# Kernel optimization log

Measured on AMD Instinct MI355X. Metric: run time of the kernel, lower is better.

## Reference

```python
import jax, jax.numpy as jnp
import numpy as np
import math

DIM = 1024
NUM_HEADS = 16
HEAD_DIM = DIM // NUM_HEADS
B, S = 2, 2048

def setup_inputs() -> dict:
    key = jax.random.key(0)
    ks = jax.random.split(key, 9)
    sc = 0.02
    return {
        "x": jax.random.normal(ks[0], (B, S, DIM), jnp.float32),
        "Wq": jax.random.normal(ks[1], (DIM, DIM), jnp.float32) * sc,
        "bq": jax.random.normal(ks[2], (DIM,), jnp.float32) * sc,
        "Wk": jax.random.normal(ks[3], (DIM, DIM), jnp.float32) * sc,
        "bk": jax.random.normal(ks[4], (DIM,), jnp.float32) * sc,
        "Wv": jax.random.normal(ks[5], (DIM, DIM), jnp.float32) * sc,
        "bv": jax.random.normal(ks[6], (DIM,), jnp.float32) * sc,
        "Wo": jax.random.normal(ks[7], (DIM, DIM), jnp.float32) * sc,
        "bo": jax.random.normal(ks[8], (DIM,), jnp.float32) * sc,
    }

def reference(x, Wq, bq, Wk, bk, Wv, bv, Wo, bo):
    b, s, d = x.shape
    h, hd = NUM_HEADS, HEAD_DIM
    # qkv projections: [B,S,D] -> [B,H,S,hd]
    def split_heads(t):
        return t.reshape(b, s, h, hd).transpose(0, 2, 1, 3)
    q = split_heads(x @ Wq + bq)
    k = split_heads(x @ Wk + bk)
    v = split_heads(x @ Wv + bv)
    # scores [B,H,S,S], scale, causal mask via where(-10000), softmax
    scores = jnp.einsum('bhqd,bhkd->bhqk', q, k) / math.sqrt(hd)
    causal = jnp.tril(jnp.ones((s, s), dtype=bool))  # [S,S]
    scores = jnp.where(causal[None, None], scores, jnp.asarray(-10000.0, scores.dtype))
    probs = jax.nn.softmax(scores, axis=-1)
    ctx = jnp.einsum('bhqk,bhkd->bhqd', probs, v)
    ctx = ctx.transpose(0, 2, 1, 3).reshape(b, s, d)
    return ctx @ Wo + bo
```

## Files before the change

### kernel.cpp

```cpp
#include <hip/hip_runtime.h>
#include <hip/hip_bf16.h>

#define DIM 1024
#define NUM_HEADS 16
#define HEAD_DIM 64
#define BATCH 2
#define SEQ 2048
#define M_ROWS (BATCH * SEQ)

typedef short bh8 __attribute__((ext_vector_type(8)));
typedef float f32x4 __attribute__((ext_vector_type(4)));
typedef float f32x16 __attribute__((ext_vector_type(16)));

#define SCALE_Q 0.18033688011116016f

#define MFMA16(a, b, c) __builtin_amdgcn_mfma_f32_16x16x32_bf16(a, b, c, 0, 0, 0)
#define MFMA32(a, b, c) __builtin_amdgcn_mfma_f32_32x32x16_bf16(a, b, c, 0, 0, 0)

#if __has_builtin(__builtin_amdgcn_exp2f)
#define EXP2F(x) __builtin_amdgcn_exp2f(x)
#else
#define EXP2F(x) exp2f(x)
#endif

__device__ __forceinline__ ushort f2bf(float f) {
    union { float f; unsigned u; } v; v.f = f;
    unsigned u = v.u;
    unsigned r = (u + 0x7FFFu + ((u >> 16) & 1u)) >> 16;
    return (ushort)r;
}

__device__ __forceinline__ unsigned cvt_pk_bf16(float lo, float hi) {
    unsigned r;
    asm("v_cvt_pk_bf16_f32 %0, %1, %2" : "=v"(r) : "v"(lo), "v"(hi));
    return r;
}

__device__ __forceinline__ void plane_swap(unsigned a, unsigned b,
                                           unsigned& o0, unsigned& o1, int h) {
#if __has_builtin(__builtin_amdgcn_permlane32_swap)
    (void)h;
    auto pr = __builtin_amdgcn_permlane32_swap(a, b, false, false);
    unsigned o[2]; __builtin_memcpy(o, &pr, 8);
    o0 = o[0]; o1 = o[1];
#else
    unsigned sa = (unsigned)__shfl_xor((int)a, 32);
    unsigned sb = (unsigned)__shfl_xor((int)b, 32);
    o0 = h ? sb : a;
    o1 = h ? b : sa;
#endif
}

__device__ __forceinline__ void async_cp16(const ushort* g, ushort* l) {
    __builtin_amdgcn_global_load_lds(
        (const __attribute__((address_space(1))) void*)(uintptr_t)g,
        (__attribute__((address_space(3))) void*)(uint32_t)(uintptr_t)l,
        16, 0, 0);
}

__global__ __launch_bounds__(256) void prep_inputs(
    const float* __restrict__ W0, const float* __restrict__ W1,
    const float* __restrict__ W2, const float* __restrict__ W3,
    const float* __restrict__ x,
    ushort* __restrict__ T0, ushort* __restrict__ T1,
    ushort* __restrict__ T2, ushort* __restrict__ T3,
    ushort* __restrict__ xb)
{
    const int z = blockIdx.z;
    const int t = threadIdx.x;
    if (z == 4) {
        int base = (blockIdx.y * 32 + blockIdx.x) * 1024 + t;
        const float4* in4 = (const float4*)x;
        ushort4* out4 = (ushort4*)xb;
        #pragma unroll
        for (int i = 0; i < 4; ++i) {
            float4 v = in4[base + i * 256];
            ushort4 o;
            o.x = f2bf(v.x); o.y = f2bf(v.y); o.z = f2bf(v.z); o.w = f2bf(v.w);
            out4[base + i * 256] = o;
        }
        return;
    }
    __shared__ float tile[32][33];
    const float* W = (z == 0) ? W0 : (z == 1) ? W1 : (z == 2) ? W2 : W3;
    ushort* Wt = (z == 0) ? T0 : (z == 1) ? T1 : (z == 2) ? T2 : T3;
    const int tx = t & 31, ty = t >> 5;
    const int k0 = blockIdx.y * 32, n0 = blockIdx.x * 32;
    #pragma unroll
    for (int i = 0; i < 4; ++i)
        tile[ty + 8 * i][tx] = W[(size_t)(k0 + ty + 8 * i) * DIM + n0 + tx];
    __syncthreads();
    #pragma unroll
    for (int i = 0; i < 4; ++i)
        Wt[(size_t)(n0 + ty + 8 * i) * DIM + k0 + tx] = f2bf(tile[tx][ty + 8 * i]);
}

#define GTM 128
#define GTN 64
#define GBK 64

__device__ __forceinline__ void gemm_core(
    const ushort* __restrict__ A, const ushort* __restrict__ Bt,
    ushort* smem, int m0, int n0, int t, f32x4 acc[4][2])
{
    ushort* As = smem;
    ushort* Bs = smem + 8192;
    const int lane = t & 63, wave = t >> 6;
    const int col = lane & 15, quad = lane >> 4;
    const int wm = (wave & 1) * 64, wn = (wave >> 1) * 32;

    for (int k0 = 0; k0 < DIM; k0 += GBK) {
        __syncthreads();
        #pragma unroll
        for (int j = 0; j < 4; ++j) {
            int C = wave * 256 + j * 64 + lane;
            int row = C >> 3;
            int lch = (C & 7) ^ (row & 7);
            async_cp16(&A[(size_t)(m0 + row) * DIM + k0 + lch * 8],
                       &As[(wave * 256 + j * 64) * 8]);
        }
        #pragma unroll
        for (int j = 0; j < 2; ++j) {
            int C = wave * 128 + j * 64 + lane;
            int row = C >> 3;
            int lch = (C & 7) ^ (row & 7);
            async_cp16(&Bt[(size_t)(n0 + row) * DIM + k0 + lch * 8],
                       &Bs[(wave * 128 + j * 64) * 8]);
        }
        __syncthreads();
        #pragma unroll
        for (int kk = 0; kk < 2; ++kk) {
            bh8 af[4], bfr[2];
            #pragma unroll
            for (int mi = 0; mi < 4; ++mi) {
                int row = wm + mi * 16 + col;
                af[mi] = *(const bh8*)&As[row * 64 + (((kk * 4 + quad) ^ (row & 7)) * 8)];
            }
            #pragma unroll
            for (int ni = 0; ni < 2; ++ni) {
                int row = wn + ni * 16 + col;
                bfr[ni] = *(const bh8*)&Bs[row * 64 + (((kk * 4 + quad) ^ (row & 7)) * 8)];
            }
            #pragma unroll
            for (int mi = 0; mi < 4; ++mi)
                #pragma unroll
                for (int ni = 0; ni < 2; ++ni)
                    acc[mi][ni] = MFMA16(af[mi], bfr[ni], acc[mi][ni]);
        }
    }
}

__global__ __launch_bounds__(256) void gemm_qkv(
    const ushort* __restrict__ A,
    const ushort* __restrict__ WqT, const ushort* __restrict__ WkT,
    const ushort* __restrict__ WvT,
    const float* __restrict__ bq, const float* __restrict__ bk,
    const float* __restrict__ bv,
    ushort* __restrict__ qo, ushort* __restrict__ ko_, ushort* __restrict__ vo)
{
    __shared__ ushort smem[12288];
    const int lin = blockIdx.x + 16 * blockIdx.y + 512 * blockIdx.z;
    const int swz = (lin & 7) * 192 + (lin >> 3);
    const int bx = swz & 15, by = (swz >> 4) & 31, z = swz >> 9;

    const ushort* Bt = (z == 0) ? WqT : (z == 1) ? WkT : WvT;
    const float* bias = (z == 0) ? bq : (z == 1) ? bk : bv;
    ushort* outp = (z == 0) ? qo : (z == 1) ? ko_ : vo;

    const int t = threadIdx.x;
    const int lane = t & 63, wave = t >> 6;
    const int col = lane & 15, quad = lane >> 4;
    const int m0 = by * GTM, n0 = bx * GTN;
    const int wm = (wave & 1) * 64, wn = (wave >> 1) * 32;
    f32x4 acc[4][2] = {};

    gemm_core(A, Bt, smem, m0, n0, t, acc);

    const int b = m0 >> 11, s0 = m0 & (SEQ - 1);
    const int h = n0 >> 6;

    if (z < 2) {
        const float scl = (z == 0) ? SCALE_Q : 1.f;
        __syncthreads();
        ushort* LT = smem;
        #pragma unroll
        for (int mi = 0; mi < 4; ++mi)
            #pragma unroll
            for (int ni = 0; ni < 2; ++ni) {
                int dl = wn + ni * 16 + col;
                float bvv = bias[n0 + dl];
                #pragma unroll
                for (int r = 0; r < 4; ++r) {
                    int ml = wm + mi * 16 + quad * 4 + r;
                    LT[ml * 72 + dl] = f2bf((acc[mi][ni][r] + bvv) * scl);
                }
            }
        __syncthreads();
        ushort* Cp = outp + (((size_t)(b * NUM_HEADS + h) * SEQ + s0) << 6);
        #pragma unroll
        for (int i = 0; i < 4; ++i) {
            int c = i * 256 + t;
            int row = c >> 3, ko = (c & 7) * 8;
            *(uint4*)&Cp[row * 64 + ko] = *(const uint4*)&LT[row * 72 + ko];
        }
    } else {
        __syncthreads();
        ushort* LT = smem;
        #pragma unroll
        for (int mi = 0; mi < 4; ++mi)
            #pragma unroll
            for (int ni = 0; ni < 2; ++ni) {
                int nl = wn + ni * 16 + col;
                float bvv = bias[n0 + nl];
                #pragma unroll
                for (int r = 0; r < 4; ++r) {
                    int ml = wm + mi * 16 + quad * 4 + r;
                    LT[nl * 136 + ml] = f2bf(acc[mi][ni][r] + bvv);
                }
            }
        __syncthreads();
        ushort* Cp = outp + (((size_t)(b * NUM_HEADS + h) * HEAD_DIM) << 11);
        #pragma unroll
        for (int i = 0; i < 4; ++i) {
            int c = i * 256 + t;
            int row = c >> 4, mo = (c & 15) * 8;
            *(uint4*)&Cp[((size_t)row << 11) + s0 + mo] = *(const uint4*)&LT[row * 136 + mo];
        }
    }
}

__global__ __launch_bounds__(256) void gemm_out(
    const ushort* __restrict__ A, const ushort* __restrict__ Bt,
    const float* __restrict__ bias, float* __restrict__ C)
{
    __shared__ ushort smem[12288];
    const int lin = blockIdx.x + 16 * blockIdx.y;
    const int swz = (lin & 7) * 64 + (lin >> 3);
    const int bx = swz & 15, by = swz >> 4;

    const int t = threadIdx.x;
    const int lane = t & 63, wave = t >> 6;
    const int col = lane & 15, quad = lane >> 4;
    const int m0 = by * GTM, n0 = bx * GTN;
    const int wm = (wave & 1) * 64, wn = (wave >> 1) * 32;
    f32x4 acc[4][2] = {};

    gemm_core(A, Bt, smem, m0, n0, t, acc);

    #pragma unroll
    for (int mi = 0; mi < 4; ++mi)
        #pragma unroll
        for (int ni = 0; ni < 2; ++ni) {
            int n = n0 + wn + ni * 16 + col;
            float bvv = bias[n];
            #pragma unroll
            for (int r = 0; r < 4; ++r) {
                int m = m0 + wm + mi * 16 + quad * 4 + r;
                C[(size_t)m * DIM + n] = acc[mi][ni][r] + bvv;
            }
        }
}

__global__ __launch_bounds__(256, 2) void attn_mfma(
    const ushort* __restrict__ Qg, const ushort* __restrict__ Kg,
    const ushort* __restrict__ Vtg, ushort* __restrict__ ctx)
{
    __shared__ char smem[34304];
    float* OA   = (float*)smem;
    float* OB   = (float*)(smem + 16640);
    float* lbuf = (float*)(smem + 33280);

    const int t = threadIdx.x;
    const int lane = t & 63, wave = t >> 6;
    const int q32 = lane & 31, h = lane >> 5;
    const int bh = blockIdx.x & 31;
    const int qt = 31 - (blockIdx.x >> 5);
    const int b = bh >> 4, hd = bh & 15;
    const int q0 = qt << 6;
    const int kw0 = wave * 32;
    const ushort* Kp = Kg + ((size_t)bh << 17);
    const ushort* Vp = Vtg + ((size_t)bh << 17);
    const ushort* Qp = Qg + ((size_t)bh << 17);

    bh8 qf[2][4];
    #pragma unroll
    for (int qti = 0; qti < 2; ++qti)
        #pragma unroll
        for (int kc = 0; kc < 4; ++kc)
            qf[qti][kc] = *(const bh8*)&Qp[((size_t)(q0 + qti * 32 + q32) << 6)
                                           + kc * 16 + h * 8];

    f32x16 O[2][2] = {};
    float l[2] = {0.f, 0.f};
    const int nIter = (q0 + 191) >> 7;

    bh8 kf_n[4], vf_n[2][2];
    #pragma unroll
    for (int kc = 0; kc < 4; ++kc)
        kf_n[kc] = *(const bh8*)&Kp[((size_t)(kw0 + q32) << 6) + kc * 16 + h * 8];
    #pragma unroll
    for (int dti = 0; dti < 2; ++dti)
        #pragma unroll
        for (int kc = 0; kc < 2; ++kc)
            vf_n[dti][kc] = *(const bh8*)&Vp[((size_t)(dti * 32 + q32) << 11)
                                             + kw0 + kc * 16 + h * 8];

    #pragma unroll 1
    for (int it = 0; it < nIter; ++it) {
        const int kb = it << 7;
        if (kb + kw0 > q0 + 63) break;

        bh8 kf[4], vf[2][2];
        #pragma unroll
        for (int kc = 0; kc < 4; ++kc) kf[kc] = kf_n[kc];
        #pragma unroll
        for (int dti = 0; dti < 2; ++dti) {
            vf[dti][0] = vf_n[dti][0]; vf[dti][1] = vf_n[dti][1];
        }

        const int kb2 = kb + 128;
        if (it + 1 < nIter) {
            #pragma unroll
            for (int kc = 0; kc < 4; ++kc)
                kf_n[kc] = *(const bh8*)&Kp[((size_t)(kb2 + kw0 + q32) << 6)
                                            + kc * 16 + h * 8];
            #pragma unroll
            for (int dti = 0; dti < 2; ++dti)
                #pragma unroll
                for (int kc = 0; kc < 2; ++kc)
                    vf_n[dti][kc] = *(const bh8*)&Vp[((size_t)(dti * 32 + q32) << 11)
                                                     + kb2 + kw0 + kc * 16 + h * 8];
        }

        f32x16 St[2] = {};
        __builtin_amdgcn_s_setprio(1);
        #pragma unroll
        for (int kc = 0; kc < 4; ++kc) {
            St[0] = MFMA32(kf[kc], qf[0][kc], St[0]);
            St[1] = MFMA32(kf[kc], qf[1][kc], St[1]);
        }
        __builtin_amdgcn_s_setprio(0);

        if (kb + kw0 + 31 > q0) {
            #pragma unroll
            for (int qti = 0; qti < 2; ++qti) {
                int q_abs = q0 + qti * 32 + q32;
                #pragma unroll
                for (int r = 0; r < 16; ++r) {
                    int key_abs = kb + kw0 + (r & 3) + ((r >> 2) << 3) + 4 * h;
                    if (key_abs > q_abs) St[qti][r] = -1e30f;
                }
            }
        }

        #pragma unroll
        for (int qti = 0; qti < 2; ++qti) {
            float p[16];
            #pragma unroll
            for (int r = 0; r < 16; ++r) p[r] = EXP2F(St[qti][r]);
            float t0 = (p[0] + p[1]) + (p[2] + p[3]);
            float t1 = (p[4] + p[5]) + (p[6] + p[7]);
            float t2 = (p[8] + p[9]) + (p[10] + p[11]);
            float t3 = (p[12] + p[13]) + (p[14] + p[15]);
            l[qti] += (t0 + t1) + (t2 + t3);

            unsigned w[8];
            #pragma unroll
            for (int m = 0; m < 8; ++m) w[m] = cvt_pk_bf16(p[2 * m], p[2 * m + 1]);
            unsigned j0, j1, j2, j3, j4, j5, j6, j7;
            plane_swap(w[0], w[2], j0, j2, h);
            plane_swap(w[1], w[3], j1, j3, h);
            plane_swap(w[4], w[6], j4, j6, h);
            plane_swap(w[5], w[7], j5, j7, h);
            union { unsigned u[4]; bh8 v; } pu0, pu1;
            pu0.u[0] = j0; pu0.u[1] = j1; pu0.u[2] = j2; pu0.u[3] = j3;
            pu1.u[0] = j4; pu1.u[1] = j5; pu1.u[2] = j6; pu1.u[3] = j7;

            __builtin_amdgcn_s_setprio(1);
            O[qti][0] = MFMA32(vf[0][0], pu0.v, O[qti][0]);
            O[qti][1] = MFMA32(vf[1][0], pu0.v, O[qti][1]);
            O[qti][0] = MFMA32(vf[0][1], pu1.v, O[qti][0]);
            O[qti][1] = MFMA32(vf[1][1], pu1.v, O[qti][1]);
            __builtin_amdgcn_s_setprio(0);
        }
    }

    l[0] += __shfl_xor(l[0], 32);
    l[1] += __shfl_xor(l[1], 32);
    if (lane < 32) {
        lbuf[wave * 64 + q32]      = l[0];
        lbuf[wave * 64 + 32 + q32] = l[1];
    }
    __syncthreads();

    if (wave == 1 || wave == 3) {
        float* dst = (wave == 1) ? OA : OB;
        #pragma unroll
        for (int qti = 0; qti < 2; ++qti)
            #pragma unroll
            for (int dti = 0; dti < 2; ++dti)
                #pragma unroll
                for (int r = 0; r < 16; ++r) {
                    int d_l = dti * 32 + (r & 3) + ((r >> 2) << 3) + 4 * h;
                    dst[d_l * 65 + qti * 32 + q32] = O[qti][dti][r];
                }
    }
    __syncthreads();
    if (wave == 0 || wave == 2) {
        float* src = (wave == 0) ? OA : OB;
        #pragma unroll
        for (int qti = 0; qti < 2; ++qti)
            #pragma unroll
            for (int dti = 0; dti < 2; ++dti)
                #pragma unroll
                for (int r = 0; r < 16; ++r) {
                    int d_l = dti * 32 + (r & 3) + ((r >> 2) << 3) + 4 * h;
                    O[qti][dti][r] += src[d_l * 65 + qti * 32 + q32];
                }
    }
    __syncthreads();
    if (wave == 2) {
        #pragma unroll
        for (int qti = 0; qti < 2; ++qti)
            #pragma unroll
            for (int dti = 0; dti < 2; ++dti)
                #pragma unroll
                for (int r = 0; r < 16; ++r) {
                    int d_l = dti * 32 + (r & 3) + ((r >> 2) << 3) + 4 * h;
                    OA[d_l * 65 + qti * 32 + q32] = O[qti][dti][r];
                }
    }
    __syncthreads();
    if (wave == 0) {
        float tot0 = lbuf[q32] + lbuf[64 + q32] + lbuf[128 + q32] + lbuf[192 + q32];
        float tot1 = lbuf[32 + q32] + lbuf[96 + q32] + lbuf[160 + q32] + lbuf[224 + q32];
        float inv0 = 1.f / tot0, inv1 = 1.f / tot1;
        ushort* Oq = (ushort*)(smem + 16640);
        #pragma unroll
        for (int qti = 0; qti < 2; ++qti) {
            float invq = qti ? inv1 : inv0;
            int qrow = qti * 32 + q32;
            #pragma unroll
            for (int dti = 0; dti < 2; ++dti)
                #pragma unroll
                for (int rg = 0; rg < 4; ++rg) {
                    int d0 = dti * 32 + rg * 8 + 4 * h;
                    float s0 = (O[qti][dti][rg * 4 + 0] + OA[(d0 + 0) * 65 + qrow]) * invq;
                    float s1 = (O[qti][dti][rg * 4 + 1] + OA[(d0 + 1) * 65 + qrow]) * invq;
                    float s2 = (O[qti][dti][rg * 4 + 2] + OA[(d0 + 2) * 65 + qrow]) * invq;
                    float s3 = (O[qti][dti][rg * 4 + 3] + OA[(d0 + 3) * 65 + qrow]) * invq;
                    uint2 pk; pk.x = cvt_pk_bf16(s0, s1); pk.y = cvt_pk_bf16(s2, s3);
                    *(uint2*)&Oq[qrow * 72 + d0] = pk;
                }
        }
        #pragma unroll
        for (int i = 0; i < 8; ++i) {
            int c = i * 64 + lane;
            int row = c >> 3, ko = (c & 7) * 8;
            *(uint4*)&ctx[((size_t)(b * SEQ) + q0 + row) * DIM + (hd << 6) + ko] =
                *(const uint4*)&Oq[row * 72 + ko];
        }
    }
}

extern "C" void kernel_launch(void* const* d_in, const int* in_sizes, int n_in,
                              void* d_out, int out_size, void* d_ws, size_t ws_size,
                              hipStream_t stream) {
    const float* x  = (const float*)d_in[0];
    const float* Wq = (const float*)d_in[1];
    const float* bq = (const float*)d_in[2];
    const float* Wk = (const float*)d_in[3];
    const float* bk = (const float*)d_in[4];
    const float* Wv = (const float*)d_in[5];
    const float* bv = (const float*)d_in[6];
    const float* Wo = (const float*)d_in[7];
    const float* bo = (const float*)d_in[8];
    float* out = (float*)d_out;

    ushort* x_bf   = (ushort*)d_ws;
    ushort* wq_t   = x_bf + 4194304;
    ushort* wk_t   = wq_t + 1048576;
    ushort* wv_t   = wk_t + 1048576;
    ushort* wo_t   = wv_t + 1048576;
    ushort* q_ws   = wo_t + 1048576;
    ushort* k_ws   = q_ws + 4194304;
    ushort* vt_ws  = k_ws + 4194304;
    ushort* ctx_ws = vt_ws + 4194304;

    dim3 pgrid(32, 32, 5);
    prep_inputs<<<pgrid, 256, 0, stream>>>(Wq, Wk, Wv, Wo, x,
                                           wq_t, wk_t, wv_t, wo_t, x_bf);

    dim3 qkv_grid(DIM / GTN, M_ROWS / GTM, 3);
    gemm_qkv<<<qkv_grid, 256, 0, stream>>>(x_bf, wq_t, wk_t, wv_t,
                                           bq, bk, bv, q_ws, k_ws, vt_ws);

    attn_mfma<<<1024, 256, 0, stream>>>(q_ws, k_ws, vt_ws, ctx_ws);

    dim3 ogrid(DIM / GTN, M_ROWS / GTM);
    gemm_out<<<ogrid, 256, 0, stream>>>(ctx_ws, wo_t, bo, out);
}
```

Measured before the change: 181.7 us.

## Fuse Q/K/V projections into one block sharing the A tile

The QKV GEMM changes from three separate block sets (one per weight) to a single 512-thread block that loads each x tile once and multiplies it against Wq, Wk and Wv tiles together. This removes the A-tile reload across the three projections, leaving one third of the blocks, each doing three times the work. The epilogue writes the three outputs one after another through shared memory. The block uses more LDS and accumulator registers and there are fewer blocks, which may lower occupancy and load balance.

```diff
diff --git a/kernel.cpp b/kernel.cpp
--- a/kernel.cpp
+++ b/kernel.cpp
@@ -95,9 +95,137 @@
         Wt[(size_t)(n0 + ty + 8 * i) * DIM + k0 + tx] = f2bf(tile[tx][ty + 8 * i]);
 }
 
+__global__ __launch_bounds__(512, 4) void gemm_qkv(
+    const ushort* __restrict__ A,
+    const ushort* __restrict__ WqT, const ushort* __restrict__ WkT,
+    const ushort* __restrict__ WvT,
+    const float* __restrict__ bq, const float* __restrict__ bk,
+    const float* __restrict__ bv,
+    ushort* __restrict__ qo, ushort* __restrict__ ko_, ushort* __restrict__ vo)
+{
+    __shared__ ushort smem[20480];
+    ushort* As  = smem;
+    ushort* Bs0 = smem + 8192;
+    ushort* Bs1 = smem + 12288;
+    ushort* Bs2 = smem + 16384;
+
+    const int lin = blockIdx.x + 16 * blockIdx.y;
+    const int swz = (lin & 7) * 64 + (lin >> 3);
+    const int bx = swz & 15, by = swz >> 4;
+
+    const int t = threadIdx.x;
+    const int lane = t & 63, wave = t >> 6;
+    const int col = lane & 15, quad = lane >> 4;
+    const int m0 = by * 128, n0 = bx * 64;
+    const int wm = (wave & 3) * 32, wn = (wave >> 2) * 32;
+
+    f32x4 acc[3][2][2] = {};
+
+    for (int k0 = 0; k0 < DIM; k0 += 64) {
+        __syncthreads();
+        #pragma unroll
+        for (int j = 0; j < 2; ++j) {
+            int C = wave * 128 + j * 64 + lane;
+            int row = C >> 3;
+            int lch = (C & 7) ^ (row & 7);
+            async_cp16(&A[(size_t)(m0 + row) * DIM + k0 + lch * 8],
+                       &As[(wave * 128 + j * 64) * 8]);
+        }
+        {
+            int C = wave * 64 + lane;
+            int row = C >> 3;
+            int lch = (C & 7) ^ (row & 7);
+            size_t goff = (size_t)(n0 + row) * DIM + k0 + lch * 8;
+            async_cp16(&WqT[goff], &Bs0[(wave * 64) * 8]);
+            async_cp16(&WkT[goff], &Bs1[(wave * 64) * 8]);
+            async_cp16(&WvT[goff], &Bs2[(wave * 64) * 8]);
+        }
+        __syncthreads();
+        #pragma unroll
+        for (int kk = 0; kk < 2; ++kk) {
+            bh8 af[2];
+            #pragma unroll
+            for (int mi = 0; mi < 2; ++mi) {
+                int row = wm + mi * 16 + col;
+                af[mi] = *(const bh8*)&As[row * 64 + (((kk * 4 + quad) ^ (row & 7)) * 8)];
+            }
+            const ushort* Bsz[3] = { Bs0, Bs1, Bs2 };
+            #pragma unroll
+            for (int z = 0; z < 3; ++z) {
+                bh8 bfr[2];
+                #pragma unroll
+                for (int ni = 0; ni < 2; ++ni) {
+                    int row = wn + ni * 16 + col;
+                    bfr[ni] = *(const bh8*)&Bsz[z][row * 64 + (((kk * 4 + quad) ^ (row & 7)) * 8)];
+                }
+                #pragma unroll
+                for (int mi = 0; mi < 2; ++mi)
+                    #pragma unroll
+                    for (int ni = 0; ni < 2; ++ni)
+                        acc[z][mi][ni] = MFMA16(af[mi], bfr[ni], acc[z][mi][ni]);
+            }
+        }
+    }
+
+    const int b = m0 >> 11, s0 = m0 & (SEQ - 1);
+    const int h = bx;
+
+    #pragma unroll 1
+    for (int z = 0; z < 3; ++z) {
+        const float* bias = (z == 0) ? bq : (z == 1) ? bk : bv;
+        ushort* outp = (z == 0) ? qo : (z == 1) ? ko_ : vo;
+        __syncthreads();
+        if (z < 2) {
+            const float scl = (z == 0) ? SCALE_Q : 1.f;
+            ushort* LT = smem;
+            #pragma unroll
+            for (int mi = 0; mi < 2; ++mi)
+                #pragma unroll
+                for (int ni = 0; ni < 2; ++ni) {
+                    int dl = wn + ni * 16 + col;
+                    float bvv = bias[n0 + dl];
+                    #pragma unroll
+                    for (int r = 0; r < 4; ++r) {
+                        int ml = wm + mi * 16 + quad * 4 + r;
+                        LT[ml * 72 + dl] = f2bf((acc[z][mi][ni][r] + bvv) * scl);
+                    }
+                }
+            __syncthreads();
+            ushort* Cp = outp + (((size_t)(b * NUM_HEADS + h) * SEQ + s0) << 6);
+            #pragma unroll
+            for (int i = 0; i < 2; ++i) {
+                int c = i * 512 + t;
+                int row = c >> 3, ko = (c & 7) * 8;
+                *(uint4*)&Cp[row * 64 + ko] = *(const uint4*)&LT[row * 72 + ko];
+            }
+        } else {
+            ushort* LT = smem;
+            #pragma unroll
+            for (int mi = 0; mi < 2; ++mi)
+                #pragma unroll
+                for (int ni = 0; ni < 2; ++ni) {
+                    int nl = wn + ni * 16 + col;
+                    float bvv = bias[n0 + nl];
+                    #pragma unroll
+                    for (int r = 0; r < 4; ++r) {
+                        int ml = wm + mi * 16 + quad * 4 + r;
+                        LT[nl * 136 + ml] = f2bf(acc[z][mi][ni][r] + bvv);
+                    }
+                }
+            __syncthreads();
+            ushort* Cp = outp + (((size_t)(b * NUM_HEADS + h) * HEAD_DIM) << 11);
+            #pragma unroll
+            for (int i = 0; i < 2; ++i) {
+                int c = i * 512 + t;
+                int row = c >> 4, mo = (c & 15) * 8;
+                *(uint4*)&Cp[((size_t)row << 11) + s0 + mo] = *(const uint4*)&LT[row * 136 + mo];
+            }
+        }
+    }
+}
+
 #define GTM 128
 #define GTN 64
-#define GBK 64
 
 __device__ __forceinline__ void gemm_core(
     const ushort* __restrict__ A, const ushort* __restrict__ Bt,
@@ -109,7 +237,7 @@
     const int col = lane & 15, quad = lane >> 4;
     const int wm = (wave & 1) * 64, wn = (wave >> 1) * 32;
 
-    for (int k0 = 0; k0 < DIM; k0 += GBK) {
+    for (int k0 = 0; k0 < DIM; k0 += 64) {
         __syncthreads();
         #pragma unroll
         for (int j = 0; j < 4; ++j) {
@@ -146,85 +274,6 @@
                 #pragma unroll
                 for (int ni = 0; ni < 2; ++ni)
                     acc[mi][ni] = MFMA16(af[mi], bfr[ni], acc[mi][ni]);
-        }
-    }
-}
-
-__global__ __launch_bounds__(256) void gemm_qkv(
-    const ushort* __restrict__ A,
-    const ushort* __restrict__ WqT, const ushort* __restrict__ WkT,
-    const ushort* __restrict__ WvT,
-    const float* __restrict__ bq, const float* __restrict__ bk,
-    const float* __restrict__ bv,
-    ushort* __restrict__ qo, ushort* __restrict__ ko_, ushort* __restrict__ vo)
-{
-    __shared__ ushort smem[12288];
-    const int lin = blockIdx.x + 16 * blockIdx.y + 512 * blockIdx.z;
-    const int swz = (lin & 7) * 192 + (lin >> 3);
-    const int bx = swz & 15, by = (swz >> 4) & 31, z = swz >> 9;
-
-    const ushort* Bt = (z == 0) ? WqT : (z == 1) ? WkT : WvT;
-    const float* bias = (z == 0) ? bq : (z == 1) ? bk : bv;
-    ushort* outp = (z == 0) ? qo : (z == 1) ? ko_ : vo;
-
-    const int t = threadIdx.x;
-    const int lane = t & 63, wave = t >> 6;
-    const int col = lane & 15, quad = lane >> 4;
-    const int m0 = by * GTM, n0 = bx * GTN;
-    const int wm = (wave & 1) * 64, wn = (wave >> 1) * 32;
-    f32x4 acc[4][2] = {};
-
-    gemm_core(A, Bt, smem, m0, n0, t, acc);
-
-    const int b = m0 >> 11, s0 = m0 & (SEQ - 1);
-    const int h = n0 >> 6;
-
-    if (z < 2) {
-        const float scl = (z == 0) ? SCALE_Q : 1.f;
-        __syncthreads();
-        ushort* LT = smem;
-        #pragma unroll
-        for (int mi = 0; mi < 4; ++mi)
-            #pragma unroll
-            for (int ni = 0; ni < 2; ++ni) {
-                int dl = wn + ni * 16 + col;
-                float bvv = bias[n0 + dl];
-                #pragma unroll
-                for (int r = 0; r < 4; ++r) {
-                    int ml = wm + mi * 16 + quad * 4 + r;
-                    LT[ml * 72 + dl] = f2bf((acc[mi][ni][r] + bvv) * scl);
-                }
-            }
-        __syncthreads();
-        ushort* Cp = outp + (((size_t)(b * NUM_HEADS + h) * SEQ + s0) << 6);
-        #pragma unroll
-        for (int i = 0; i < 4; ++i) {
-            int c = i * 256 + t;
-            int row = c >> 3, ko = (c & 7) * 8;
-            *(uint4*)&Cp[row * 64 + ko] = *(const uint4*)&LT[row * 72 + ko];
-        }
-    } else {
-        __syncthreads();
-        ushort* LT = smem;
-        #pragma unroll
-        for (int mi = 0; mi < 4; ++mi)
-            #pragma unroll
-            for (int ni = 0; ni < 2; ++ni) {
-                int nl = wn + ni * 16 + col;
-                float bvv = bias[n0 + nl];
-                #pragma unroll
-                for (int r = 0; r < 4; ++r) {
-                    int ml = wm + mi * 16 + quad * 4 + r;
-                    LT[nl * 136 + ml] = f2bf(acc[mi][ni][r] + bvv);
-                }
-            }
-        __syncthreads();
-        ushort* Cp = outp + (((size_t)(b * NUM_HEADS + h) * HEAD_DIM) << 11);
-        #pragma unroll
-        for (int i = 0; i < 4; ++i) {
-            int c = i * 256 + t;
-            int row = c >> 4, mo = (c & 15) * 8;
-            *(uint4*)&Cp[((size_t)row << 11) + s0 + mo] = *(const uint4*)&LT[row * 136 + mo];
         }
     }
 }
@@ -491,8 +540,8 @@
     prep_inputs<<<pgrid, 256, 0, stream>>>(Wq, Wk, Wv, Wo, x,
                                            wq_t, wk_t, wv_t, wo_t, x_bf);
 
-    dim3 qkv_grid(DIM / GTN, M_ROWS / GTM, 3);
-    gemm_qkv<<<qkv_grid, 256, 0, stream>>>(x_bf, wq_t, wk_t, wv_t,
+    dim3 qkv_grid(16, 32);
+    gemm_qkv<<<qkv_grid, 512, 0, stream>>>(x_bf, wq_t, wk_t, wv_t,
                                            bq, bk, bv, q_ws, k_ws, vt_ws);
 
     attn_mfma<<<1024, 256, 0, stream>>>(q_ws, k_ws, vt_ws, ctx_ws);
```

Measured after the change: 394.1 us. +116.9%, slower.
